# Optimization experiments

Hardware: AMD Instinct MI355X
Metric: run time of the kernel (lower is better)

The kernel has to match this reference:

```python
import jax, jax.numpy as jnp
import numpy as np

B, S, D, H, WS = 2, 4096, 768, 12, 256
HD = D // H
NW = S // WS
EPS = 1e-5


def layernorm(x, g, b):
    mu = jnp.mean(x, axis=-1, keepdims=True)
    var = jnp.mean(jnp.square(x - mu), axis=-1, keepdims=True)
    return (x - mu) * jax.lax.rsqrt(var + EPS) * g + b


def setup_inputs() -> dict:
    key = jax.random.key(0)
    ks = jax.random.split(key, 8)
    s = 0.02
    return {
        "x": jax.random.normal(ks[0], (B, S, D), dtype=jnp.float32),
        "Wq": jax.random.normal(ks[1], (D, D), dtype=jnp.float32) * s,
        "bq": jnp.zeros((D,), jnp.float32),
        "Wk": jax.random.normal(ks[2], (D, D), dtype=jnp.float32) * s,
        "bk": jnp.zeros((D,), jnp.float32),
        "Wv": jax.random.normal(ks[3], (D, D), dtype=jnp.float32) * s,
        "bv": jnp.zeros((D,), jnp.float32),
        "Wo": jax.random.normal(ks[4], (D, D), dtype=jnp.float32) * s,
        "bo": jnp.zeros((D,), jnp.float32),
        "ln1_g": jnp.ones((D,), jnp.float32),
        "ln1_b": jnp.zeros((D,), jnp.float32),
        "W1": jax.random.normal(ks[5], (D, 4 * D), dtype=jnp.float32) * s,
        "b1": jnp.zeros((4 * D,), jnp.float32),
        "W2": jax.random.normal(ks[6], (4 * D, D), dtype=jnp.float32) * s,
        "b2": jnp.zeros((D,), jnp.float32),
        "ln2_g": jnp.ones((D,), jnp.float32),
        "ln2_b": jnp.zeros((D,), jnp.float32),
    }


def _attn(h, Wq, bq, Wk, bk, Wv, bv, Wo, bo):
    q = (h @ Wq + bq).reshape(B, S, H, HD)
    k = (h @ Wk + bk).reshape(B, S, H, HD)
    v = (h @ Wv + bv).reshape(B, S, H, HD)
    # split into windows: [B, NW, WS, H, HD]
    kb = k.reshape(B, NW, WS, H, HD)
    vb = v.reshape(B, NW, WS, H, HD)
    qw = jnp.moveaxis(q.reshape(B, NW, WS, H, HD), 1, 0)  # [NW, B, WS, H, HD]
    inv = 1.0 / np.sqrt(HD).astype(np.float32)

    def step(carry, qi_i):
        qi, i = qi_i  # qi: [B, WS, H, HD]
        # per key-window scores: [B, H, NW, WSq, WSk]
        scores = jnp.einsum('bqhd,bjkhd->bhjqk', qi, kb) * inv
        attn = jax.nn.softmax(scores, axis=-1)  # per-block softmax (as in source)
        mask = (jnp.arange(NW) <= i).astype(attn.dtype)  # block-causal, include own window
        attn = attn * mask[None, None, :, None, None]
        ctx = jnp.einsum('bhjqk,bjkhd->bqhd', attn, vb)  # sum over key windows
        return carry, ctx

    _, ctxs = jax.lax.scan(step, None, (qw, jnp.arange(NW)))
    ctx = jnp.moveaxis(ctxs, 0, 1).reshape(B, S, D)
    return ctx @ Wo + bo


def reference(x, Wq, bq, Wk, bk, Wv, bv, Wo, bo, ln1_g, ln1_b, W1, b1, W2, b2, ln2_g, ln2_b):
    attn_out = _attn(layernorm(x, ln1_g, ln1_b), Wq, bq, Wk, bk, Wv, bv, Wo, bo)
    x = x + attn_out
    h2 = layernorm(x, ln2_g, ln2_b)
    ff = jax.nn.gelu(h2 @ W1 + b1, approximate=False) @ W2 + b2
    return x + ff
```

## Files before the change

kernel.cpp:

```cpp
#include <hip/hip_runtime.h>
#include <cstdint>
#include <cstddef>

#define DEV __device__ __forceinline__

typedef unsigned short u16;
typedef unsigned int u32;
typedef __attribute__((ext_vector_type(8))) short s16x8;
typedef __attribute__((ext_vector_type(4))) float f32x4;

typedef unsigned int u32_as1 __attribute__((address_space(1)));
typedef unsigned int u32_as3 __attribute__((address_space(3)));

DEV u16 f2bf(float f){
  unsigned u = __float_as_uint(f);
  u += 0x7fffu + ((u >> 16) & 1u);
  return (u16)(u >> 16);
}

DEV u32 cvtpk_bf16(float lo, float hi){
  u32 r;
  asm("v_cvt_pk_bf16_f32 %0, %1, %2" : "=v"(r) : "v"(lo), "v"(hi));
  return r;
}

DEV void gload16(const void* g, void* l){
  __builtin_amdgcn_global_load_lds((const u32_as1*)g, (u32_as3*)l, 16, 0, 0);
}

__global__ __launch_bounds__(256) void wconv_kernel(const float* __restrict__ W,
                                                    u16* __restrict__ Wt, int K, int N){
  __shared__ float tl[32][33];
  int tx = threadIdx.x & 31, ty = threadIdx.x >> 5;
  int k0 = blockIdx.x * 32, n0 = blockIdx.y * 32;
  #pragma unroll
  for (int p=0;p<4;p++)
    tl[ty+8*p][tx] = W[(size_t)(k0+ty+8*p)*N + (n0+tx)];
  __syncthreads();
  #pragma unroll
  for (int p=0;p<4;p++){
    int n = ty+8*p;
    Wt[(size_t)(n0+n)*K + (k0+tx)] = f2bf(tl[tx][n]);
  }
}

__global__ __launch_bounds__(256) void vconv_kernel(const u16* __restrict__ vbuf,
                                                    u16* __restrict__ vtb){
  int t = threadIdx.x;
  int kt = blockIdx.x, bh = blockIdx.y;
  int b = bh / 12, h = bh - b*12;
  int d = t & 63, kg = t >> 6;
  const u16* src = vbuf + ((size_t)(b*4096 + kt*64) * 768) + h*64 + d;
  u16* dst = vtb + ((size_t)bh*64 + d)*4096 + kt*64;
  #pragma unroll
  for (int j=0;j<2;j++){
    int kc = kg*2 + j;
    s16x8 o;
    #pragma unroll
    for (int e=0;e<8;e++){
      int klocal = (kc>>2)*32 + 4*(kc&3) + (e>>1) + 16*(e&1);
      ((u16*)&o)[e] = src[(size_t)klocal*768];
    }
    *(s16x8*)(dst + kc*8) = o;
  }
}

__global__ __launch_bounds__(256) void ln_kernel(const float* __restrict__ x,
                                                 const float* __restrict__ g,
                                                 const float* __restrict__ bta,
                                                 u16* __restrict__ out){
  int row = blockIdx.x, t = threadIdx.x;
  const float* xr = x + (size_t)row*768;
  float v0 = xr[t], v1 = xr[t+256], v2 = xr[t+512];
  float s = v0+v1+v2, s2 = v0*v0+v1*v1+v2*v2;
  #pragma unroll
  for (int m=1;m<64;m<<=1){ s += __shfl_xor(s,m); s2 += __shfl_xor(s2,m); }
  __shared__ float ls[4], ls2[4];
  int w = t>>6;
  if ((t&63)==0){ ls[w]=s; ls2[w]=s2; }
  __syncthreads();
  s = ls[0]+ls[1]+ls[2]+ls[3]; s2 = ls2[0]+ls2[1]+ls2[2]+ls2[3];
  float mu = s*(1.0f/768.0f);
  float rstd = rsqrtf(s2*(1.0f/768.0f) - mu*mu + 1e-5f);
  u16* orow = out + (size_t)row*768;
  orow[t]     = f2bf((v0-mu)*rstd*g[t]     + bta[t]);
  orow[t+256] = f2bf((v1-mu)*rstd*g[t+256] + bta[t+256]);
  orow[t+512] = f2bf((v2-mu)*rstd*g[t+512] + bta[t+512]);
}

template<bool GELU, bool RES, bool OUTBF16, int BM>
__global__ __launch_bounds__(256) void gemm_kernel(
    const u16* __restrict__ A, const u16* __restrict__ Bt0, size_t btStride,
    const float* __restrict__ bias0, const float* __restrict__ bias1, const float* __restrict__ bias2,
    const float* __restrict__ res, void* __restrict__ out0, size_t outStride,
    int M, int N, int K, float qscale)
{
  constexpr int AM = BM/32;
  __shared__ u16 As[BM*64];
  __shared__ u16 Bs[128*64];
  const int t = threadIdx.x, lane = t & 63, w = t >> 6;
  const int lj = lane & 15, g = lane >> 4;
  const int wm = w >> 1, wn = w & 1;
  const int z = blockIdx.z;
  const u16* Bt = Bt0 + (size_t)z * btStride;
  const float* bias = (z==0) ? bias0 : (z==1 ? bias1 : bias2);
  const u16* Arow = A  + (size_t)blockIdx.x * BM * K;
  const u16* Brow = Bt + (size_t)blockIdx.y * 128 * K;

  f32x4 acc[AM][4];
  #pragma unroll
  for (int a=0;a<AM;a++)
    #pragma unroll
    for (int b=0;b<4;b++){ f32x4 zz = {0.f,0.f,0.f,0.f}; acc[a][b] = zz; }

  for (int kk=0; kk<K; kk+=64){
    #pragma unroll
    for (int cc=0;cc<BM/32;cc++){
      int c = cc*256 + t;
      int row = c>>3, gp = c&7;
      gload16(Arow + (size_t)row*K + kk + ((gp ^ (row&7))<<3),
              (void*)(As + (size_t)(cc*256 + w*64)*8));
    }
    #pragma unroll
    for (int cc=0;cc<4;cc++){
      int c = cc*256 + t;
      int row = c>>3, gp = c&7;
      gload16(Brow + (size_t)row*K + kk + ((gp ^ (row&7))<<3),
              (void*)(Bs + (size_t)(cc*256 + w*64)*8));
    }
    __syncthreads();
    #pragma unroll
    for (int ks=0;ks<2;ks++){
      s16x8 af[AM], bfr[4];
      #pragma unroll
      for (int mt=0;mt<AM;mt++){
        int row = wm*(BM/2)+mt*16+lj;
        af[mt]  = *(const s16x8*)&As[(size_t)row*64 + (((ks*4+g) ^ (lj&7))<<3)];
      }
      #pragma unroll
      for (int nt=0;nt<4;nt++){
        int row = wn*64+nt*16+lj;
        bfr[nt] = *(const s16x8*)&Bs[(size_t)row*64 + (((ks*4+g) ^ (lj&7))<<3)];
      }
      #pragma unroll
      for (int mt=0;mt<AM;mt++)
        #pragma unroll
        for (int nt=0;nt<4;nt++)
          acc[mt][nt] = __builtin_amdgcn_mfma_f32_16x16x32_bf16(af[mt], bfr[nt], acc[mt][nt], 0,0,0);
    }
    __syncthreads();
  }

  const size_t gr0 = (size_t)blockIdx.x*BM + wm*(BM/2);
  const int gc0 = blockIdx.y*128 + wn*64;
  float* outF = (float*)out0; u16* outB = (u16*)out0;
  if (OUTBF16) outB += (size_t)z*outStride; else outF += (size_t)z*outStride;
  #pragma unroll
  for (int mt=0;mt<AM;mt++)
    #pragma unroll
    for (int nt=0;nt<4;nt++){
      int gc = gc0 + nt*16 + lj;
      float bv = bias[gc];
      #pragma unroll
      for (int r=0;r<4;r++){
        size_t gr = gr0 + mt*16 + g*4 + r;
        float val = acc[mt][nt][r] + bv;
        if (z==0) val *= qscale;
        if (RES)  val += res[gr*(size_t)N + gc];
        if (GELU) val = 0.5f*val*(1.0f + erff(val*0.70710678118f));
        if (OUTBF16) outB[gr*(size_t)N + gc] = f2bf(val);
        else         outF[gr*(size_t)N + gc] = val;
      }
    }
}

__global__ __launch_bounds__(256,3) void attn_kernel(
    const u16* __restrict__ qb, const u16* __restrict__ kb,
    const u16* __restrict__ vtb, u16* __restrict__ ctx)
{
  __shared__ u16 KV[256*64];
  __shared__ u32 Ps[4][16*20];
  const int t = threadIdx.x, lane = t & 63, w = t >> 6;
  const int lj = lane & 15, g = lane >> 4;
  const int bx = blockIdx.x;
  const int pp = bx & 7, qq = (bx >> 3) & 3, bh = bx >> 5;
  const int h = bh % 12, b = bh / 12;
  const size_t seqbase = (size_t)b * 4096;
  const int hoff = h * 64;

  #pragma unroll
  for (int f=0; f<2; f++){
    const int iw = f ? (15 - pp) : pp;
    const int qrow0 = iw*256 + qq*64 + w*16;

    s16x8 qa[2];
    #pragma unroll
    for (int ks=0;ks<2;ks++)
      qa[ks] = *(const s16x8*)(qb + (seqbase + qrow0 + lj)*768 + hoff + ks*32 + g*8);

    f32x4 cacc[4];
    #pragma unroll
    for (int dt=0;dt<4;dt++){ f32x4 zz = {0.f,0.f,0.f,0.f}; cacc[dt] = zz; }

    for (int jw=0; jw<=iw; jw++){
      const u16* kwin = kb + (seqbase + jw*256)*768 + hoff;
      const u16* vtwin = vtb + (size_t)bh*64*4096 + jw*256;

      __syncthreads();
      #pragma unroll
      for (int cc=0;cc<8;cc++){
        int c = cc*256 + t;
        int krow = c>>3, vp = c&7;
        gload16(kwin + (size_t)krow*768 + ((vp ^ (krow&7))<<3),
                (void*)(KV + (size_t)(cc*256 + w*64)*8));
      }
      __syncthreads();

      f32x4 sacc[16];
      #pragma unroll
      for (int kt=0;kt<16;kt++){ f32x4 zz = {0.f,0.f,0.f,0.f}; sacc[kt] = zz; }
      __builtin_amdgcn_s_setprio(1);
      #pragma unroll
      for (int kt=0;kt<16;kt++){
        int kl = kt*16 + lj;
        #pragma unroll
        for (int ks=0;ks<2;ks++){
          s16x8 kf = *(const s16x8*)&KV[ (size_t)kl*64 + (((4*ks+g) ^ (kl&7))<<3) ];
          sacc[kt] = __builtin_amdgcn_mfma_f32_16x16x32_bf16(qa[ks], kf, sacc[kt], 0,0,0);
        }
      }
      __builtin_amdgcn_s_setprio(0);
      __syncthreads();

      #pragma unroll
      for (int cc=0;cc<8;cc++){
        int c = cc*256 + t;
        int d = c>>5, cp = c&31;
        gload16(vtwin + (size_t)d*4096 + ((cp ^ (d&15))<<3),
                (void*)(KV + (size_t)(cc*256 + w*64)*8));
      }

      float sm[4], rs[4];
      #pragma unroll
      for (int r=0;r<4;r++) sm[r] = 0.f;
      #pragma unroll
      for (int kt=0;kt<16;kt++)
        #pragma unroll
        for (int r=0;r<4;r++){
          float pv = exp2f(sacc[kt][r]);
          sacc[kt][r] = pv; sm[r] += pv;
        }
      #pragma unroll
      for (int msk=1; msk<16; msk<<=1)
        #pragma unroll
        for (int r=0;r<4;r++) sm[r] += __shfl_xor(sm[r], msk);
      #pragma unroll
      for (int r=0;r<4;r++) rs[r] = 1.0f / sm[r];

      __syncthreads();

      #pragma unroll
      for (int ks=0;ks<8;ks++){
        #pragma unroll
        for (int r=0;r<4;r++)
          Ps[w][ (4*g+r)*20 + lj ] = cvtpk_bf16(sacc[2*ks][r]*rs[r], sacc[2*ks+1][r]*rs[r]);
        s16x8 pa = *(const s16x8*)&Ps[w][ lj*20 + g*4 ];
        __builtin_amdgcn_s_setprio(1);
        #pragma unroll
        for (int dt=0;dt<4;dt++){
          int d = dt*16 + lj;
          s16x8 vf = *(const s16x8*)&KV[ (size_t)d*256 + (((4*ks+g) ^ (d&15))<<3) ];
          cacc[dt] = __builtin_amdgcn_mfma_f32_16x16x32_bf16(pa, vf, cacc[dt], 0,0,0);
        }
        __builtin_amdgcn_s_setprio(0);
      }
    }

    #pragma unroll
    for (int dt=0;dt<4;dt++)
      #pragma unroll
      for (int r=0;r<4;r++){
        int qrow = qrow0 + g*4 + r;
        ctx[ (seqbase + qrow)*768 + hoff + dt*16 + lj ] = f2bf(cacc[dt][r]);
      }
  }
}

extern "C" void kernel_launch(void* const* d_in, const int* in_sizes, int n_in,
                              void* d_out, int out_size, void* d_ws, size_t ws_size,
                              hipStream_t stream)
{
  const float* x    = (const float*)d_in[0];
  const float* Wq   = (const float*)d_in[1];
  const float* bq   = (const float*)d_in[2];
  const float* Wk   = (const float*)d_in[3];
  const float* bk   = (const float*)d_in[4];
  const float* Wv   = (const float*)d_in[5];
  const float* bv   = (const float*)d_in[6];
  const float* Wo   = (const float*)d_in[7];
  const float* bo   = (const float*)d_in[8];
  const float* ln1g = (const float*)d_in[9];
  const float* ln1b = (const float*)d_in[10];
  const float* W1   = (const float*)d_in[11];
  const float* b1   = (const float*)d_in[12];
  const float* W2   = (const float*)d_in[13];
  const float* b2   = (const float*)d_in[14];
  const float* ln2g = (const float*)d_in[15];
  const float* ln2b = (const float*)d_in[16];

  char* ws = (char*)d_ws;
  constexpr size_t SZ_W768  = (size_t)768*768*2;
  constexpr size_t SZ_W3072 = (size_t)768*3072*2;
  constexpr size_t SZ_HB    = (size_t)8192*768*2;
  u16* wtq = (u16*)(ws);
  u16* wtk = (u16*)(ws + SZ_W768);
  u16* wtv = (u16*)(ws + 2*SZ_W768);
  u16* wto = (u16*)(ws + 3*SZ_W768);
  u16* wt1 = (u16*)(ws + 4*SZ_W768);
  u16* wt2 = (u16*)(ws + 4*SZ_W768 + SZ_W3072);
  char* p0 = ws + 4*SZ_W768 + 2*SZ_W3072;
  u16*   hbuf = (u16*)p0;
  u16*   qbuf = (u16*)(p0 + SZ_HB);
  u16*   kbuf = (u16*)(p0 + 2*SZ_HB);
  u16*   vbuf = (u16*)(p0 + 3*SZ_HB);
  u16*   cbuf = (u16*)(p0 + 4*SZ_HB);
  float* x1   = (float*)(p0 + 5*SZ_HB);
  u16*   vtbuf = hbuf;
  u16*   ffa  = qbuf;
  float* outp = (float*)d_out;

  wconv_kernel<<<dim3(24,24), 256, 0, stream>>>(Wq, wtq, 768, 768);
  wconv_kernel<<<dim3(24,24), 256, 0, stream>>>(Wk, wtk, 768, 768);
  wconv_kernel<<<dim3(24,24), 256, 0, stream>>>(Wv, wtv, 768, 768);
  wconv_kernel<<<dim3(24,24), 256, 0, stream>>>(Wo, wto, 768, 768);
  wconv_kernel<<<dim3(24,96), 256, 0, stream>>>(W1, wt1, 768, 3072);
  wconv_kernel<<<dim3(96,24), 256, 0, stream>>>(W2, wt2, 3072, 768);

  ln_kernel<<<8192, 256, 0, stream>>>(x, ln1g, ln1b, hbuf);
  gemm_kernel<false,false,true,128><<<dim3(64,6,3), 256, 0, stream>>>(
      hbuf, wtq, (size_t)768*768, bq, bk, bv, nullptr, qbuf, (size_t)8192*768,
      8192, 768, 768, 0.180336880111f);
  vconv_kernel<<<dim3(64,24), 256, 0, stream>>>(vbuf, vtbuf);
  attn_kernel<<<768, 256, 0, stream>>>(qbuf, kbuf, vtbuf, cbuf);
  gemm_kernel<false,true,false,64><<<dim3(128,6,1), 256, 0, stream>>>(
      cbuf, wto, 0, bo, bo, bo, x, x1, 0, 8192, 768, 768, 1.0f);
  ln_kernel<<<8192, 256, 0, stream>>>(x1, ln2g, ln2b, hbuf);
  gemm_kernel<true,false,true,128><<<dim3(64,24,1), 256, 0, stream>>>(
      hbuf, wt1, 0, b1, b1, b1, nullptr, ffa, 0, 8192, 3072, 768, 1.0f);
  gemm_kernel<false,true,false,64><<<dim3(128,6,1), 256, 0, stream>>>(
      ffa, wt2, 0, b2, b2, b2, x1, outp, 0, 8192, 768, 3072, 1.0f);
}
```

Baseline: 330.9 us.

## Read K fragments from global directly, stage V transpose via LDS, batch weight conversions

```diff
diff --git a/kernel.cpp b/kernel.cpp
--- a/kernel.cpp
+++ b/kernel.cpp
@@ -28,9 +28,16 @@
   __builtin_amdgcn_global_load_lds((const u32_as1*)g, (u32_as3*)l, 16, 0, 0);
 }
 
-__global__ __launch_bounds__(256) void wconv_kernel(const float* __restrict__ W,
-                                                    u16* __restrict__ Wt, int K, int N){
+template<int NZ>
+__global__ __launch_bounds__(256) void wconv_kernel(
+    const float* __restrict__ Wa, const float* __restrict__ Wb,
+    const float* __restrict__ Wc, const float* __restrict__ Wd,
+    u16* __restrict__ Da, u16* __restrict__ Db, u16* __restrict__ Dc, u16* __restrict__ Dd,
+    int K, int N){
   __shared__ float tl[32][33];
+  int z = (NZ>1) ? blockIdx.z : 0;
+  const float* W = (z==0)?Wa:(z==1)?Wb:(z==2)?Wc:Wd;
+  u16* Wt = (z==0)?Da:(z==1)?Db:(z==2)?Dc:Dd;
   int tx = threadIdx.x & 31, ty = threadIdx.x >> 5;
   int k0 = blockIdx.x * 32, n0 = blockIdx.y * 32;
   #pragma unroll
@@ -46,22 +53,30 @@
 
 __global__ __launch_bounds__(256) void vconv_kernel(const u16* __restrict__ vbuf,
                                                     u16* __restrict__ vtb){
+  __shared__ u16 TL[64][65];
   int t = threadIdx.x;
   int kt = blockIdx.x, bh = blockIdx.y;
   int b = bh / 12, h = bh - b*12;
+  const u16* src = vbuf + ((size_t)(b*4096 + kt*64) * 768) + h*64;
   int d = t & 63, kg = t >> 6;
-  const u16* src = vbuf + ((size_t)(b*4096 + kt*64) * 768) + h*64 + d;
-  u16* dst = vtb + ((size_t)bh*64 + d)*4096 + kt*64;
-  #pragma unroll
-  for (int j=0;j<2;j++){
-    int kc = kg*2 + j;
+  #pragma unroll
+  for (int j=0;j<16;j++){
+    int k = kg*16 + j;
+    TL[k][d] = src[(size_t)k*768 + d];
+  }
+  __syncthreads();
+  u16* dst = vtb + ((size_t)bh*64)*4096 + (size_t)kt*64;
+  #pragma unroll
+  for (int it=0; it<2; it++){
+    int idx = it*256 + t;
+    int dd = idx >> 3, gn = idx & 7;
     s16x8 o;
     #pragma unroll
     for (int e=0;e<8;e++){
-      int klocal = (kc>>2)*32 + 4*(kc&3) + (e>>1) + 16*(e&1);
-      ((u16*)&o)[e] = src[(size_t)klocal*768];
-    }
-    *(s16x8*)(dst + kc*8) = o;
+      int klocal = (gn>>2)*32 + 4*(gn&3) + (e>>1) + 16*(e&1);
+      ((u16*)&o)[e] = TL[klocal][dd];
+    }
+    *(s16x8*)(dst + (size_t)dd*4096 + gn*8) = o;
   }
 }
 
@@ -178,7 +193,7 @@
     const u16* __restrict__ qb, const u16* __restrict__ kb,
     const u16* __restrict__ vtb, u16* __restrict__ ctx)
 {
-  __shared__ u16 KV[256*64];
+  __shared__ u16 Vs[64*256];
   __shared__ u32 Ps[4][16*20];
   const int t = threadIdx.x, lane = t & 63, w = t >> 6;
   const int lj = lane & 15, g = lane >> 4;
@@ -210,35 +225,24 @@
       #pragma unroll
       for (int cc=0;cc<8;cc++){
         int c = cc*256 + t;
-        int krow = c>>3, vp = c&7;
-        gload16(kwin + (size_t)krow*768 + ((vp ^ (krow&7))<<3),
-                (void*)(KV + (size_t)(cc*256 + w*64)*8));
-      }
-      __syncthreads();
-
-      f32x4 sacc[16];
-      #pragma unroll
-      for (int kt=0;kt<16;kt++){ f32x4 zz = {0.f,0.f,0.f,0.f}; sacc[kt] = zz; }
-      __builtin_amdgcn_s_setprio(1);
-      #pragma unroll
-      for (int kt=0;kt<16;kt++){
-        int kl = kt*16 + lj;
-        #pragma unroll
-        for (int ks=0;ks<2;ks++){
-          s16x8 kf = *(const s16x8*)&KV[ (size_t)kl*64 + (((4*ks+g) ^ (kl&7))<<3) ];
-          sacc[kt] = __builtin_amdgcn_mfma_f32_16x16x32_bf16(qa[ks], kf, sacc[kt], 0,0,0);
-        }
-      }
-      __builtin_amdgcn_s_setprio(0);
-      __syncthreads();
-
-      #pragma unroll
-      for (int cc=0;cc<8;cc++){
-        int c = cc*256 + t;
         int d = c>>5, cp = c&31;
         gload16(vtwin + (size_t)d*4096 + ((cp ^ (d&15))<<3),
-                (void*)(KV + (size_t)(cc*256 + w*64)*8));
-      }
+                (void*)(Vs + (size_t)(cc*256 + w*64)*8));
+      }
+
+      f32x4 sacc[16];
+      #pragma unroll
+      for (int kt=0;kt<16;kt++){ f32x4 zz = {0.f,0.f,0.f,0.f}; sacc[kt] = zz; }
+      const u16* kbase = kwin + (size_t)lj*768 + g*8;
+      __builtin_amdgcn_s_setprio(1);
+      #pragma unroll
+      for (int kt=0;kt<16;kt++){
+        s16x8 kf0 = *(const s16x8*)(kbase + (size_t)kt*16*768);
+        s16x8 kf1 = *(const s16x8*)(kbase + (size_t)kt*16*768 + 32);
+        sacc[kt] = __builtin_amdgcn_mfma_f32_16x16x32_bf16(qa[0], kf0, sacc[kt], 0,0,0);
+        sacc[kt] = __builtin_amdgcn_mfma_f32_16x16x32_bf16(qa[1], kf1, sacc[kt], 0,0,0);
+      }
+      __builtin_amdgcn_s_setprio(0);
 
       float sm[4], rs[4];
       #pragma unroll
@@ -269,7 +273,7 @@
         #pragma unroll
         for (int dt=0;dt<4;dt++){
           int d = dt*16 + lj;
-          s16x8 vf = *(const s16x8*)&KV[ (size_t)d*256 + (((4*ks+g) ^ (d&15))<<3) ];
+          s16x8 vf = *(const s16x8*)&Vs[ (size_t)d*256 + (((4*ks+g) ^ (d&15))<<3) ];
           cacc[dt] = __builtin_amdgcn_mfma_f32_16x16x32_bf16(pa, vf, cacc[dt], 0,0,0);
         }
         __builtin_amdgcn_s_setprio(0);
@@ -329,12 +333,12 @@
   u16*   ffa  = qbuf;
   float* outp = (float*)d_out;
 
-  wconv_kernel<<<dim3(24,24), 256, 0, stream>>>(Wq, wtq, 768, 768);
-  wconv_kernel<<<dim3(24,24), 256, 0, stream>>>(Wk, wtk, 768, 768);
-  wconv_kernel<<<dim3(24,24), 256, 0, stream>>>(Wv, wtv, 768, 768);
-  wconv_kernel<<<dim3(24,24), 256, 0, stream>>>(Wo, wto, 768, 768);
-  wconv_kernel<<<dim3(24,96), 256, 0, stream>>>(W1, wt1, 768, 3072);
-  wconv_kernel<<<dim3(96,24), 256, 0, stream>>>(W2, wt2, 3072, 768);
+  wconv_kernel<4><<<dim3(24,24,4), 256, 0, stream>>>(
+      Wq, Wk, Wv, Wo, wtq, wtk, wtv, wto, 768, 768);
+  wconv_kernel<1><<<dim3(24,96), 256, 0, stream>>>(
+      W1, W1, W1, W1, wt1, wt1, wt1, wt1, 768, 3072);
+  wconv_kernel<1><<<dim3(96,24), 256, 0, stream>>>(
+      W2, W2, W2, W2, wt2, wt2, wt2, wt2, 3072, 768);
 
   ln_kernel<<<8192, 256, 0, stream>>>(x, ln1g, ln1b, hbuf);
   gemm_kernel<false,false,true,128><<<dim3(64,6,3), 256, 0, stream>>>(
```

Result: slower. 436.1 us (+31.8%).
